# Kernel optimization log

Hardware: AMD Instinct MI355X
Metric: run time of the kernel (lower is better)

Reference implementation:

```python
import jax, jax.numpy as jnp
import numpy as np

# PGA G(3,0,1) blade basis, standard ordering
BLADES = [(), (0,), (1,), (2,), (3,), (0,1), (0,2), (0,3), (1,2), (1,3), (2,3),
          (0,1,2), (0,1,3), (0,2,3), (1,2,3), (0,1,2,3)]
IDX = {b: i for i, b in enumerate(BLADES)}
METRIC = (0, 1, 1, 1)  # e0^2 = 0, e1^2 = e2^2 = e3^2 = 1


def _mul(a, b, wedge=False):
    """Product of basis blades; returns (sign, blade) with sign 0 if vanishing."""
    s = list(a) + list(b)
    sign = 1
    changed = True
    while changed:  # bubble sort, counting swaps
        changed = False
        for i in range(len(s) - 1):
            if s[i] > s[i + 1]:
                s[i], s[i + 1] = s[i + 1], s[i]
                sign = -sign
                changed = True
    out, i = [], 0
    while i < len(s):
        if i + 1 < len(s) and s[i] == s[i + 1]:
            if wedge:
                return 0, None
            sign *= METRIC[s[i]]
            i += 2
        else:
            out.append(s[i]); i += 1
    if sign == 0:
        return 0, None
    return sign, tuple(out)


def _build_cayley(wedge):
    C = np.zeros((16, 16, 16), np.float32)
    for i, a in enumerate(BLADES):
        for j, b in enumerate(BLADES):
            s, r = _mul(a, b, wedge=wedge)
            if s:
                C[i, j, IDX[r]] = s
    return C


def _build_dual():
    """dual(x) = D @ x with a ^ dual(a) = e0123."""
    D = np.zeros((16, 16), np.float32)
    full = (0, 1, 2, 3)
    for i, a in enumerate(BLADES):
        comp = tuple(x for x in full if x not in a)
        s, r = _mul(a, comp, wedge=True)
        assert r == full
        D[IDX[comp], i] = s
    return D


def _build_basis():
    """9 equivariant linear basis maps: 5 grade projections + 4 e0-multiplications."""
    maps = []
    for g in range(5):
        M = np.zeros((16, 16), np.float32)
        for i, b in enumerate(BLADES):
            if len(b) == g:
                M[i, i] = 1.0
        maps.append(M)
    for g in range(4):
        M = np.zeros((16, 16), np.float32)
        for i, b in enumerate(BLADES):
            if len(b) == g and 0 not in b:
                s, r = _mul((0,), b)
                M[IDX[r], i] = s
        maps.append(M)
    return np.stack(maps)  # [9, 16, 16]


_GP = jnp.asarray(_build_cayley(False))
_WEDGE = jnp.asarray(_build_cayley(True))
_DUAL_NP = _build_dual()
_DUAL = jnp.asarray(_DUAL_NP)
_UNDUAL = jnp.asarray(np.linalg.inv(_DUAL_NP).astype(np.float32))
_BASIS = jnp.asarray(_build_basis())


def equi_linear(x, w):
    # x: [B, P, in, 16], w: [out, in, 9] -> [B, P, out, 16]
    wk = jnp.einsum('oib,bkl->oikl', w, _BASIS)
    return jnp.einsum('oikl,BPil->BPok', wk, x)


def geometric_product(x, y):
    return jnp.einsum('ijk,BPci,BPcj->BPck', _GP, x, y)


def equi_join(x, y, ref):
    dx = jnp.einsum('kl,BPcl->BPck', _DUAL, x)
    dy = jnp.einsum('kl,BPcl->BPck', _DUAL, y)
    w = jnp.einsum('ijk,BPci,BPcj->BPck', _WEDGE, dx, dy)
    j = jnp.einsum('kl,BPcl->BPck', _UNDUAL, w)
    return j * ref[..., 15:16]  # scale by reference pseudoscalar (equivariance fix)


def setup_inputs() -> dict:
    key = jax.random.key(0)
    k1, k2, k3, k4 = jax.random.split(key, 4)
    B, P, C_hidden, C_inter = 64, 1024, 48, 48
    hidden = jax.random.normal(k1, (B, P, C_hidden, 16), dtype=jnp.float32)
    ref = jax.random.normal(k2, (B, 1, 1, 16), dtype=jnp.float32)
    scale_b = 1.0 / np.sqrt(C_hidden * 9)
    scale_n = 1.0 / np.sqrt(C_inter * 9)
    w_bili = jax.random.normal(k3, (2 * C_inter, C_hidden, 9), dtype=jnp.float32) * scale_b
    w_next = jax.random.normal(k4, (C_hidden, C_inter, 9), dtype=jnp.float32) * scale_n
    return {"hidden": hidden, "ref": ref, "w_bili": w_bili, "w_next": w_next}


def reference(hidden, ref, w_bili, w_next):
    h = equi_linear(hidden, w_bili)              # [B, P, 96, 16]
    lg, rg, lj, rj = jnp.split(h, 4, axis=-2)    # each [B, P, 24, 16]
    gp = geometric_product(lg, rg)
    jn = equi_join(lj, rj, ref)
    out = jnp.concatenate([gp, jn], axis=-2)     # [B, P, 48, 16]
    return equi_linear(out, w_next)
```

## Files before the change

### kernel.cpp

```cpp
#include <hip/hip_runtime.h>


constexpr unsigned char BB[16] = {
  0x0, 0x1, 0x2, 0x4, 0x8,
  0x3, 0x5, 0x9, 0x6, 0xA, 0xC,
  0x7, 0xB, 0xD, 0xE,
  0xF
};
constexpr int popc4(unsigned x){ return (x&1)+((x>>1)&1)+((x>>2)&1)+((x>>3)&1); }
constexpr int idx_of(unsigned bits){
  int r = 0;
  for (int i = 0; i < 16; ++i) if (BB[i] == bits) r = i;
  return r;
}
constexpr int reorder_sign(unsigned a, unsigned b){
  int sw = 0;
  for (int g = 0; g < 4; ++g) if (b & (1u<<g)) sw += popc4(a >> (g+1));
  return (sw & 1) ? -1 : 1;
}
struct Tab { signed char s[16][16]; signed char k[16][16]; };
constexpr Tab make_gp(){
  Tab t{};
  for (int i = 0; i < 16; ++i)
    for (int j = 0; j < 16; ++j){
      unsigned a = BB[i], b = BB[j];
      if ((a & b) & 1u) { t.s[i][j] = 0; t.k[i][j] = 0; }
      else { t.s[i][j] = (signed char)reorder_sign(a,b);
             t.k[i][j] = (signed char)idx_of(a ^ b); }
    }
  return t;
}
constexpr int d_idx(int i){ return idx_of(0xFu ^ BB[i]); }
constexpr int d_sgn(int i){ return reorder_sign(BB[i], 0xFu ^ BB[i]); }
constexpr Tab make_join(){
  Tab t{};
  for (int a = 0; a < 16; ++a)
    for (int b = 0; b < 16; ++b){
      int da = d_idx(a), db = d_idx(b);
      if (BB[da] & BB[db]) { t.s[a][b] = 0; t.k[a][b] = 0; }
      else {
        int ws = reorder_sign(BB[da], BB[db]);
        int m  = idx_of(BB[da] ^ BB[db]);
        int l  = idx_of(0xFu ^ BB[m]);
        t.s[a][b] = (signed char)(d_sgn(a) * d_sgn(b) * ws * d_sgn(l));
        t.k[a][b] = (signed char)l;
      }
    }
  return t;
}
constexpr Tab GPT = make_gp();
constexpr Tab JNT = make_join();

struct ITab { int v[16]; };
constexpr ITab make_grade(){ ITab t{}; for (int i=0;i<16;++i) t.v[i]=popc4(BB[i]); return t; }
constexpr ITab make_partner(){ ITab t{}; for (int i=0;i<16;++i) t.v[i]=idx_of(BB[i] & ~1u); return t; }
constexpr ITab make_e0(){ ITab t{}; for (int i=0;i<16;++i) t.v[i]=(BB[i]&1u); return t; }
constexpr ITab GRD = make_grade();
constexpr ITab PRT = make_partner();
constexpr ITab E0T = make_e0();

#define NPTS   65536
#define CIN    48
#define CH     96
#define COUT   48
#define PTS    8
#define XROWF  772
#define WSTR   432

__device__ __forceinline__ float f4c(const float4& v, int c){
  return c==0 ? v.x : (c==1 ? v.y : (c==2 ? v.z : v.w));
}

__global__ void prep_weights(const float* __restrict__ wb,
                             const float* __restrict__ wn,
                             float* __restrict__ W1, float* __restrict__ W2){
  int i = blockIdx.x * 256 + threadIdx.x;
  if (i < 9*CH*CIN){
    int o = i / WSTR; int r = i % WSTR; int b = r / CIN; int c = r % CIN;
    W1[i] = wb[(o*CIN + c)*9 + b];
  }
  if (i < 9*COUT*CIN){
    int o = i / WSTR; int r = i % WSTR; int b = r / CIN; int c = r % CIN;
    W2[i] = wn[(o*CIN + c)*9 + b];
  }
}

__global__ __launch_bounds__(256, 3)
void fused_bilinear(const float* __restrict__ x,
                    const float* __restrict__ refp,
                    const float* __restrict__ W1,
                    const float* __restrict__ W2,
                    float* __restrict__ out){
  __shared__ float xs[PTS * XROWF];
  __shared__ float gs[PTS * XROWF];

  const int t  = threadIdx.x;
  const long p0 = (long)blockIdx.x * PTS;

  for (int c = t; c < PTS * 192; c += 256){
    int p = c / 192, r = c % 192;
    ((float4*)(xs + p * XROWF))[r] = ((const float4*)(x + (p0 + p) * 768))[r];
  }
  __syncthreads();

  for (int tau = t; tau < PTS * 48; tau += 256){
    const int p = tau & (PTS - 1);
    const int c = tau >> 3;
    const int cl = (c < 24) ? c        : (24 + c);
    const int cr = (c < 24) ? (24 + c) : (48 + c);
    const float* __restrict__ Wl = W1 + cl * WSTR;
    const float* __restrict__ Wr = W1 + cr * WSTR;

    float hl[16], hr[16];
    #pragma unroll
    for (int k = 0; k < 16; ++k){ hl[k] = 0.f; hr[k] = 0.f; }

    #pragma unroll 1
    for (int i0 = 0; i0 < CIN; i0 += 4){
      float4 wl[9], wr[9];
      #pragma unroll
      for (int b = 0; b < 9; ++b){
        wl[b] = *(const float4*)(Wl + b*CIN + i0);
        wr[b] = *(const float4*)(Wr + b*CIN + i0);
      }
      #pragma unroll
      for (int di = 0; di < 4; ++di){
        const float* xi = xs + p * XROWF + (i0 + di) * 16;
        const float4 x0 = *(const float4*)(xi);
        const float4 x1 = *(const float4*)(xi + 4);
        const float4 x2 = *(const float4*)(xi + 8);
        const float4 x3 = *(const float4*)(xi + 12);
        const float xv[16] = {x0.x,x0.y,x0.z,x0.w, x1.x,x1.y,x1.z,x1.w,
                              x2.x,x2.y,x2.z,x2.w, x3.x,x3.y,x3.z,x3.w};
        #pragma unroll
        for (int k = 0; k < 16; ++k){
          const float xk = xv[k];
          hl[k] += f4c(wl[GRD.v[k]], di) * xk;
          hr[k] += f4c(wr[GRD.v[k]], di) * xk;
        }
        #pragma unroll
        for (int k = 0; k < 16; ++k){
          if (E0T.v[k]){
            const float xp = xv[PRT.v[k]];
            hl[k] += f4c(wl[4 + GRD.v[k]], di) * xp;
            hr[k] += f4c(wr[4 + GRD.v[k]], di) * xp;
          }
        }
      }
    }

    float oo[16];
    #pragma unroll
    for (int k = 0; k < 16; ++k) oo[k] = 0.f;
    if (c < 24){
      #pragma unroll
      for (int i = 0; i < 16; ++i)
        #pragma unroll
        for (int j = 0; j < 16; ++j){
          const int s = GPT.s[i][j];
          if (s > 0)      oo[GPT.k[i][j]] += hl[i]*hr[j];
          else if (s < 0) oo[GPT.k[i][j]] -= hl[i]*hr[j];
        }
    } else {
      #pragma unroll
      for (int i = 0; i < 16; ++i)
        #pragma unroll
        for (int j = 0; j < 16; ++j){
          const int s = JNT.s[i][j];
          if (s > 0)      oo[JNT.k[i][j]] += hl[i]*hr[j];
          else if (s < 0) oo[JNT.k[i][j]] -= hl[i]*hr[j];
        }
      const float rps = refp[(int)((p0 + p) >> 10) * 16 + 15];
      #pragma unroll
      for (int k = 0; k < 16; ++k) oo[k] *= rps;
    }
    float* gp_ = gs + p * XROWF + c * 16;
    *(float4*)(gp_ + 0)  = make_float4(oo[0], oo[1], oo[2], oo[3]);
    *(float4*)(gp_ + 4)  = make_float4(oo[4], oo[5], oo[6], oo[7]);
    *(float4*)(gp_ + 8)  = make_float4(oo[8], oo[9], oo[10],oo[11]);
    *(float4*)(gp_ + 12) = make_float4(oo[12],oo[13],oo[14],oo[15]);
  }
  __syncthreads();

  float* outS = xs;
  for (int tau = t; tau < PTS * 48; tau += 256){
    const int p = tau & (PTS - 1);
    const int o = tau >> 3;
    const float* __restrict__ Wo = W2 + o * WSTR;

    float acc[16];
    #pragma unroll
    for (int k = 0; k < 16; ++k) acc[k] = 0.f;

    #pragma unroll 1
    for (int c0 = 0; c0 < CIN; c0 += 4){
      float4 w[9];
      #pragma unroll
      for (int b = 0; b < 9; ++b) w[b] = *(const float4*)(Wo + b*CIN + c0);
      #pragma unroll
      for (int dc = 0; dc < 4; ++dc){
        const float* gi = gs + p * XROWF + (c0 + dc) * 16;
        const float4 g0 = *(const float4*)(gi);
        const float4 g1 = *(const float4*)(gi + 4);
        const float4 g2 = *(const float4*)(gi + 8);
        const float4 g3 = *(const float4*)(gi + 12);
        const float gv[16] = {g0.x,g0.y,g0.z,g0.w, g1.x,g1.y,g1.z,g1.w,
                              g2.x,g2.y,g2.z,g2.w, g3.x,g3.y,g3.z,g3.w};
        #pragma unroll
        for (int k = 0; k < 16; ++k)
          acc[k] += f4c(w[GRD.v[k]], dc) * gv[k];
        #pragma unroll
        for (int k = 0; k < 16; ++k){
          if (E0T.v[k])
            acc[k] += f4c(w[4 + GRD.v[k]], dc) * gv[PRT.v[k]];
        }
      }
    }
    float* op_ = outS + p * XROWF + o * 16;
    *(float4*)(op_ + 0)  = make_float4(acc[0], acc[1], acc[2], acc[3]);
    *(float4*)(op_ + 4)  = make_float4(acc[4], acc[5], acc[6], acc[7]);
    *(float4*)(op_ + 8)  = make_float4(acc[8], acc[9], acc[10],acc[11]);
    *(float4*)(op_ + 12) = make_float4(acc[12],acc[13],acc[14],acc[15]);
  }
  __syncthreads();

  for (int c = t; c < PTS * 192; c += 256){
    int p = c / 192, r = c % 192;
    ((float4*)(out + (p0 + p) * 768))[r] = ((const float4*)(outS + p * XROWF))[r];
  }
}

extern "C" void kernel_launch(void* const* d_in, const int* in_sizes, int n_in,
                              void* d_out, int out_size, void* d_ws, size_t ws_size,
                              hipStream_t stream){
  (void)in_sizes; (void)n_in; (void)out_size; (void)ws_size;
  const float* hidden = (const float*)d_in[0];
  const float* refp   = (const float*)d_in[1];
  const float* wbili  = (const float*)d_in[2];
  const float* wnext  = (const float*)d_in[3];
  float* outp = (float*)d_out;

  float* W1 = (float*)d_ws;
  float* W2 = W1 + 9*CH*CIN;

  prep_weights<<<162, 256, 0, stream>>>(wbili, wnext, W1, W2);
  fused_bilinear<<<NPTS/PTS, 256, 0, stream>>>(hidden, refp, W1, W2, outp);
}
```

Before: 2.152 ms.

## Remap threads to per-component linear maps and split bilinear into two phases

Threads now work on one (point, blade component, output half) each. Every thread caches the 48 input values for its component, and its partner component for e0 blades, in registers, then computes the equivariant linear layers as 48-wide dot products. Weights are re-laid out basis-major so each thread streams contiguous rows. The geometric product and join run as separate phases, each followed by a barrier, and only the first half of the threads do the bilinear work, which adds load imbalance. The e0 threads do twice the work of the free ones, and the larger register arrays risk lower occupancy.

Result: slower. 7.872 ms (+265.8%).

```diff
diff --git a/kernel.cpp b/kernel.cpp
--- a/kernel.cpp
+++ b/kernel.cpp
@@ -54,36 +54,108 @@
 struct ITab { int v[16]; };
 constexpr ITab make_grade(){ ITab t{}; for (int i=0;i<16;++i) t.v[i]=popc4(BB[i]); return t; }
 constexpr ITab make_partner(){ ITab t{}; for (int i=0;i<16;++i) t.v[i]=idx_of(BB[i] & ~1u); return t; }
-constexpr ITab make_e0(){ ITab t{}; for (int i=0;i<16;++i) t.v[i]=(BB[i]&1u); return t; }
 constexpr ITab GRD = make_grade();
 constexpr ITab PRT = make_partner();
-constexpr ITab E0T = make_e0();
+constexpr int KPERM[16] = {0,2,3,4,8,9,10,14,  1,5,6,7,11,12,13,15};
 
 #define NPTS   65536
 #define CIN    48
 #define CH     96
 #define COUT   48
 #define PTS    8
-#define XROWF  772
-#define WSTR   432
-
-__device__ __forceinline__ float f4c(const float4& v, int c){
-  return c==0 ? v.x : (c==1 ? v.y : (c==2 ? v.z : v.w));
-}
+#define ROWF   772
 
 __global__ void prep_weights(const float* __restrict__ wb,
                              const float* __restrict__ wn,
                              float* __restrict__ W1, float* __restrict__ W2){
   int i = blockIdx.x * 256 + threadIdx.x;
   if (i < 9*CH*CIN){
-    int o = i / WSTR; int r = i % WSTR; int b = r / CIN; int c = r % CIN;
+    int b = i / (CH*CIN); int r = i % (CH*CIN); int o = r / CIN; int c = r % CIN;
     W1[i] = wb[(o*CIN + c)*9 + b];
   }
   if (i < 9*COUT*CIN){
-    int o = i / WSTR; int r = i % WSTR; int b = r / CIN; int c = r % CIN;
+    int b = i / (COUT*CIN); int r = i % (COUT*CIN); int o = r / CIN; int c = r % CIN;
     W2[i] = wn[(o*CIN + c)*9 + b];
   }
 }
+
+#define LD16(dst, base) { \
+  float4 q0_ = *(const float4*)((base)+0);  float4 q1_ = *(const float4*)((base)+4); \
+  float4 q2_ = *(const float4*)((base)+8);  float4 q3_ = *(const float4*)((base)+12); \
+  dst[0]=q0_.x;  dst[1]=q0_.y;  dst[2]=q0_.z;  dst[3]=q0_.w; \
+  dst[4]=q1_.x;  dst[5]=q1_.y;  dst[6]=q1_.z;  dst[7]=q1_.w; \
+  dst[8]=q2_.x;  dst[9]=q2_.y;  dst[10]=q2_.z; dst[11]=q2_.w; \
+  dst[12]=q3_.x; dst[13]=q3_.y; dst[14]=q3_.z; dst[15]=q3_.w; }
+
+#define ST16(base, src) { \
+  *(float4*)((base)+0)  = make_float4(src[0], src[1], src[2], src[3]); \
+  *(float4*)((base)+4)  = make_float4(src[4], src[5], src[6], src[7]); \
+  *(float4*)((base)+8)  = make_float4(src[8], src[9], src[10],src[11]); \
+  *(float4*)((base)+12) = make_float4(src[12],src[13],src[14],src[15]); }
+
+#define DO_LIN1(HA) do { \
+  const int ob_ = (HA)*48 + oh*24; \
+  if (isfree){ \
+    const float* wpl_ = W1 + g*(CH*CIN) + ob_*CIN; \
+    _Pragma("unroll 2") \
+    for (int j = 0; j < 24; ++j){ \
+      const float* wr_ = wpl_ + j*CIN; \
+      float a0=0.f,a1=0.f,a2=0.f,a3=0.f; \
+      _Pragma("unroll") \
+      for (int i = 0; i < 48; i += 4){ \
+        float4 wv = *(const float4*)(wr_ + i); \
+        a0 += wv.x*xr[i];   a1 += wv.y*xr[i+1]; \
+        a2 += wv.z*xr[i+2]; a3 += wv.w*xr[i+3]; \
+      } \
+      Hs[p*ROWF + (oh*24+j)*16 + k] = (a0+a1)+(a2+a3); \
+    } \
+  } else { \
+    const float* wplA_ = W1 + g*(CH*CIN) + ob_*CIN; \
+    const float* wplB_ = W1 + (4+g)*(CH*CIN) + ob_*CIN; \
+    _Pragma("unroll 1") \
+    for (int j = 0; j < 24; ++j){ \
+      const float* wrA_ = wplA_ + j*CIN; \
+      const float* wrB_ = wplB_ + j*CIN; \
+      float a0=0.f,a1=0.f,a2=0.f,a3=0.f; \
+      _Pragma("unroll") \
+      for (int i = 0; i < 48; i += 4){ \
+        float4 wv  = *(const float4*)(wrA_ + i); \
+        float4 wv2 = *(const float4*)(wrB_ + i); \
+        a0 += wv.x*xr[i];     a1 += wv.y*xr[i+1]; \
+        a2 += wv.z*xr[i+2];   a3 += wv.w*xr[i+3]; \
+        a0 += wv2.x*xr2[i];   a1 += wv2.y*xr2[i+1]; \
+        a2 += wv2.z*xr2[i+2]; a3 += wv2.w*xr2[i+3]; \
+      } \
+      Hs[p*ROWF + (oh*24+j)*16 + k] = (a0+a1)+(a2+a3); \
+    } \
+  } \
+} while(0)
+
+#define DO_BILIN(JOIN, RPS) do { \
+  if (isfree){ \
+    const int fid_ = oh*64 + s*8 + p; \
+    for (int u_ = fid_; u_ < 192; u_ += 128){ \
+      const int pp_ = u_ & 7, c_ = u_ >> 3; \
+      const float* hb_ = Hs + pp_*ROWF + c_*16; \
+      float A[16], Bv[16], oo[16]; \
+      LD16(A, hb_); LD16(Bv, hb_ + 384); \
+      _Pragma("unroll") for (int kk = 0; kk < 16; ++kk) oo[kk] = 0.f; \
+      _Pragma("unroll") \
+      for (int ii = 0; ii < 16; ++ii){ \
+        _Pragma("unroll") \
+        for (int jj = 0; jj < 16; ++jj){ \
+          const int sg_ = (JOIN) ? (int)JNT.s[ii][jj] : (int)GPT.s[ii][jj]; \
+          const int kk_ = (JOIN) ? (int)JNT.k[ii][jj] : (int)GPT.k[ii][jj]; \
+          if (sg_ > 0)      oo[kk_] += A[ii]*Bv[jj]; \
+          else if (sg_ < 0) oo[kk_] -= A[ii]*Bv[jj]; \
+        } \
+      } \
+      if (JOIN){ _Pragma("unroll") for (int kk = 0; kk < 16; ++kk) oo[kk] *= (RPS); } \
+      float* gw_ = Gs + pp_*ROWF + ((JOIN)*24 + c_)*16; \
+      ST16(gw_, oo); \
+    } \
+  } \
+} while(0)
 
 __global__ __launch_bounds__(256, 3)
 void fused_bilinear(const float* __restrict__ x,
@@ -91,142 +163,98 @@
                     const float* __restrict__ W1,
                     const float* __restrict__ W2,
                     float* __restrict__ out){
-  __shared__ float xs[PTS * XROWF];
-  __shared__ float gs[PTS * XROWF];
+  __shared__ float Hs[PTS * ROWF];
+  __shared__ float Gs[PTS * ROWF];
 
   const int t  = threadIdx.x;
   const long p0 = (long)blockIdx.x * PTS;
 
+  const int p  = t & 7;
+  const int s  = (t >> 3) & 15;
+  const int oh = t >> 7;
+  const int k  = KPERM[s];
+  const int g  = GRD.v[k];
+  const bool isfree = (s < 8);
+
   for (int c = t; c < PTS * 192; c += 256){
-    int p = c / 192, r = c % 192;
-    ((float4*)(xs + p * XROWF))[r] = ((const float4*)(x + (p0 + p) * 768))[r];
-  }
-  __syncthreads();
-
-  for (int tau = t; tau < PTS * 48; tau += 256){
-    const int p = tau & (PTS - 1);
-    const int c = tau >> 3;
-    const int cl = (c < 24) ? c        : (24 + c);
-    const int cr = (c < 24) ? (24 + c) : (48 + c);
-    const float* __restrict__ Wl = W1 + cl * WSTR;
-    const float* __restrict__ Wr = W1 + cr * WSTR;
-
-    float hl[16], hr[16];
+    int pp = c / 192, r = c % 192;
+    ((float4*)(Gs + pp * ROWF))[r] = ((const float4*)(x + (p0 + pp) * 768))[r];
+  }
+  __syncthreads();
+
+  float xr[48], xr2[48];
+  #pragma unroll
+  for (int i = 0; i < 48; ++i) xr[i] = Gs[p*ROWF + i*16 + k];
+  if (!isfree){
+    const int kp = PRT.v[k];
     #pragma unroll
-    for (int k = 0; k < 16; ++k){ hl[k] = 0.f; hr[k] = 0.f; }
-
+    for (int i = 0; i < 48; ++i) xr2[i] = Gs[p*ROWF + i*16 + kp];
+  }
+
+  const float rps = refp[(int)(p0 >> 10) * 16 + 15];
+
+  DO_LIN1(0);
+  __syncthreads();
+
+  DO_BILIN(0, 0.f);
+  __syncthreads();
+
+  DO_LIN1(1);
+  __syncthreads();
+
+  DO_BILIN(1, rps);
+  __syncthreads();
+
+  float gr[48], gr2[48];
+  #pragma unroll
+  for (int c = 0; c < 48; ++c) gr[c] = Gs[p*ROWF + c*16 + k];
+  if (!isfree){
+    const int kp = PRT.v[k];
+    #pragma unroll
+    for (int c = 0; c < 48; ++c) gr2[c] = Gs[p*ROWF + c*16 + kp];
+  }
+
+  if (isfree){
+    const float* wpl = W2 + g*(COUT*CIN);
+    #pragma unroll 2
+    for (int j = 0; j < 24; ++j){
+      const int o = oh*24 + j;
+      const float* wr_ = wpl + o*CIN;
+      float a0=0.f,a1=0.f,a2=0.f,a3=0.f;
+      #pragma unroll
+      for (int c = 0; c < 48; c += 4){
+        float4 wv = *(const float4*)(wr_ + c);
+        a0 += wv.x*gr[c];   a1 += wv.y*gr[c+1];
+        a2 += wv.z*gr[c+2]; a3 += wv.w*gr[c+3];
+      }
+      Hs[p*ROWF + o*16 + k] = (a0+a1)+(a2+a3);
+    }
+  } else {
+    const float* wplA = W2 + g*(COUT*CIN);
+    const float* wplB = W2 + (4+g)*(COUT*CIN);
     #pragma unroll 1
-    for (int i0 = 0; i0 < CIN; i0 += 4){
-      float4 wl[9], wr[9];
+    for (int j = 0; j < 24; ++j){
+      const int o = oh*24 + j;
+      const float* wrA_ = wplA + o*CIN;
+      const float* wrB_ = wplB + o*CIN;
+      float a0=0.f,a1=0.f,a2=0.f,a3=0.f;
       #pragma unroll
-      for (int b = 0; b < 9; ++b){
-        wl[b] = *(const float4*)(Wl + b*CIN + i0);
-        wr[b] = *(const float4*)(Wr + b*CIN + i0);
+      for (int c = 0; c < 48; c += 4){
+        float4 wv  = *(const float4*)(wrA_ + c);
+        float4 wv2 = *(const float4*)(wrB_ + c);
+        a0 += wv.x*gr[c];     a1 += wv.y*gr[c+1];
+        a2 += wv.z*gr[c+2];   a3 += wv.w*gr[c+3];
+        a0 += wv2.x*gr2[c];   a1 += wv2.y*gr2[c+1];
+        a2 += wv2.z*gr2[c+2]; a3 += wv2.w*gr2[c+3];
       }
-      #pragma unroll
-      for (int di = 0; di < 4; ++di){
-        const float* xi = xs + p * XROWF + (i0 + di) * 16;
-        const float4 x0 = *(const float4*)(xi);
-        const float4 x1 = *(const float4*)(xi + 4);
-        const float4 x2 = *(const float4*)(xi + 8);
-        const float4 x3 = *(const float4*)(xi + 12);
-        const float xv[16] = {x0.x,x0.y,x0.z,x0.w, x1.x,x1.y,x1.z,x1.w,
-                              x2.x,x2.y,x2.z,x2.w, x3.x,x3.y,x3.z,x3.w};
-        #pragma unroll
-        for (int k = 0; k < 16; ++k){
-          const float xk = xv[k];
-          hl[k] += f4c(wl[GRD.v[k]], di) * xk;
-          hr[k] += f4c(wr[GRD.v[k]], di) * xk;
-        }
-        #pragma unroll
-        for (int k = 0; k < 16; ++k){
-          if (E0T.v[k]){
-            const float xp = xv[PRT.v[k]];
-            hl[k] += f4c(wl[4 + GRD.v[k]], di) * xp;
-            hr[k] += f4c(wr[4 + GRD.v[k]], di) * xp;
-          }
-        }
-      }
-    }
-
-    float oo[16];
-    #pragma unroll
-    for (int k = 0; k < 16; ++k) oo[k] = 0.f;
-    if (c < 24){
-      #pragma unroll
-      for (int i = 0; i < 16; ++i)
-        #pragma unroll
-        for (int j = 0; j < 16; ++j){
-          const int s = GPT.s[i][j];
-          if (s > 0)      oo[GPT.k[i][j]] += hl[i]*hr[j];
-          else if (s < 0) oo[GPT.k[i][j]] -= hl[i]*hr[j];
-        }
-    } else {
-      #pragma unroll
-      for (int i = 0; i < 16; ++i)
-        #pragma unroll
-        for (int j = 0; j < 16; ++j){
-          const int s = JNT.s[i][j];
-          if (s > 0)      oo[JNT.k[i][j]] += hl[i]*hr[j];
-          else if (s < 0) oo[JNT.k[i][j]] -= hl[i]*hr[j];
-        }
-      const float rps = refp[(int)((p0 + p) >> 10) * 16 + 15];
-      #pragma unroll
-      for (int k = 0; k < 16; ++k) oo[k] *= rps;
-    }
-    float* gp_ = gs + p * XROWF + c * 16;
-    *(float4*)(gp_ + 0)  = make_float4(oo[0], oo[1], oo[2], oo[3]);
-    *(float4*)(gp_ + 4)  = make_float4(oo[4], oo[5], oo[6], oo[7]);
-    *(float4*)(gp_ + 8)  = make_float4(oo[8], oo[9], oo[10],oo[11]);
-    *(float4*)(gp_ + 12) = make_float4(oo[12],oo[13],oo[14],oo[15]);
-  }
-  __syncthreads();
-
-  float* outS = xs;
-  for (int tau = t; tau < PTS * 48; tau += 256){
-    const int p = tau & (PTS - 1);
-    const int o = tau >> 3;
-    const float* __restrict__ Wo = W2 + o * WSTR;
-
-    float acc[16];
-    #pragma unroll
-    for (int k = 0; k < 16; ++k) acc[k] = 0.f;
-
-    #pragma unroll 1
-    for (int c0 = 0; c0 < CIN; c0 += 4){
-      float4 w[9];
-      #pragma unroll
-      for (int b = 0; b < 9; ++b) w[b] = *(const float4*)(Wo + b*CIN + c0);
-      #pragma unroll
-      for (int dc = 0; dc < 4; ++dc){
-        const float* gi = gs + p * XROWF + (c0 + dc) * 16;
-        const float4 g0 = *(const float4*)(gi);
-        const float4 g1 = *(const float4*)(gi + 4);
-        const float4 g2 = *(const float4*)(gi + 8);
-        const float4 g3 = *(const float4*)(gi + 12);
-        const float gv[16] = {g0.x,g0.y,g0.z,g0.w, g1.x,g1.y,g1.z,g1.w,
-                              g2.x,g2.y,g2.z,g2.w, g3.x,g3.y,g3.z,g3.w};
-        #pragma unroll
-        for (int k = 0; k < 16; ++k)
-          acc[k] += f4c(w[GRD.v[k]], dc) * gv[k];
-        #pragma unroll
-        for (int k = 0; k < 16; ++k){
-          if (E0T.v[k])
-            acc[k] += f4c(w[4 + GRD.v[k]], dc) * gv[PRT.v[k]];
-        }
-      }
-    }
-    float* op_ = outS + p * XROWF + o * 16;
-    *(float4*)(op_ + 0)  = make_float4(acc[0], acc[1], acc[2], acc[3]);
-    *(float4*)(op_ + 4)  = make_float4(acc[4], acc[5], acc[6], acc[7]);
-    *(float4*)(op_ + 8)  = make_float4(acc[8], acc[9], acc[10],acc[11]);
-    *(float4*)(op_ + 12) = make_float4(acc[12],acc[13],acc[14],acc[15]);
+      Hs[p*ROWF + o*16 + k] = (a0+a1)+(a2+a3);
+    }
   }
   __syncthreads();
 
   for (int c = t; c < PTS * 192; c += 256){
-    int p = c / 192, r = c % 192;
-    ((float4*)(out + (p0 + p) * 768))[r] = ((const float4*)(outS + p * XROWF))[r];
+    int pp = c / 192, r = c % 192;
+    ((float4*)(out + (p0 + pp) * 768))[r] = ((const float4*)(Hs + pp * ROWF))[r];
   }
 }
 
```
